# Optimization experiments

Hardware: AMD Instinct MI355X
Metric: run time of the kernel (lower is better)

## Reference

```python
import jax, jax.numpy as jnp
import numpy as np

N = 50000   # nodes
R = 50      # relations
B = 30      # bases
F_IN = 64   # input features
H = 64      # hidden channels
C = 8       # classes
E = 1000000 # edges


def setup_inputs() -> dict:
    key = jax.random.key(0)
    ks = jax.random.split(key, 16)
    x = jax.random.normal(ks[0], (N, F_IN), jnp.float32)
    edge_index = jax.random.randint(ks[1], (2, E), 0, N)
    edge_type = jax.random.randint(ks[2], (E,), 0, R)
    inp = {"x": x, "edge_index": edge_index, "edge_type": edge_type}
    dims = [(F_IN, H), (H, H), (H, C)]
    i = 3
    for l, (din, dout) in enumerate(dims):
        s = 1.0 / np.sqrt(din)
        inp[f"bases{l}"] = jax.random.normal(ks[i], (B, din, dout), jnp.float32) * s; i += 1
        inp[f"comp{l}"] = jax.random.normal(ks[i], (R, B), jnp.float32) / np.sqrt(B); i += 1
        inp[f"root{l}"] = jax.random.normal(ks[i], (din, dout), jnp.float32) * s; i += 1
        inp[f"bias{l}"] = jnp.zeros((dout,), jnp.float32); i += 1
    return inp


def _rgcn(x, bases, comp, root, bias, src, seg):
    # Per-relation mean aggregation (PyG RGCNConv default aggr='mean'):
    # segment id = dst * R + relation. Mean of source features per (dst, rel),
    # then basis-decomposed transform (linearity lets transform follow the mean).
    din = x.shape[1]
    sums = jax.ops.segment_sum(x[src], seg, num_segments=N * R)          # [N*R, din]
    cnt = jax.ops.segment_sum(jnp.ones((seg.shape[0],), x.dtype), seg, num_segments=N * R)
    inv = jnp.where(cnt > 0, 1.0 / jnp.maximum(cnt, 1.0), 0.0)
    agg = (sums * inv[:, None]).reshape(N, R, din)                        # [N, R, din]
    t = jnp.einsum('nri,rb->nbi', agg, comp)                              # [N, B, din]
    msg = jnp.einsum('nbi,bio->no', t, bases)                             # [N, dout]
    return msg + x @ root + bias


def reference(x, edge_index, edge_type,
              bases0, comp0, root0, bias0,
              bases1, comp1, root1, bias1,
              bases2, comp2, root2, bias2):
    src, dst = edge_index[0], edge_index[1]
    seg = dst * R + edge_type
    params = [(bases0, comp0, root0, bias0),
              (bases1, comp1, root1, bias1),
              (bases2, comp2, root2, bias2)]
    x1 = x
    for b, c, r, bi in params:
        x1 = _rgcn(x, b, c, r, bi, src, seg)
        x = jax.nn.relu(x1)
    # original returns log_softmax of the last conv's pre-ReLU output
    return jax.nn.log_softmax(x1, axis=1)
```

## Files before the change

### kernel.cpp

```cpp
#include <hip/hip_runtime.h>
#include <hip/hip_bf16.h>
#include <hip/hip_fp16.h>
#include <stdint.h>

#define NN   50000
#define RR   50
#define BB   30
#define DIN  64
#define EE   1000000
#define KTOT (BB*DIN + DIN)
#define NBW  16
#define ROWE (KTOT + 8)
#define CPAD 32
#define EPAD (EE + 8*NN + 32)

typedef __attribute__((ext_vector_type(8))) short short8;
typedef __attribute__((ext_vector_type(4))) float floatx4;

#define RFL(x) __builtin_amdgcn_readfirstlane(x)


__global__ void k_hist(const int* __restrict__ dst, const int* __restrict__ et,
                       int* __restrict__ cnt) {
    int e = blockIdx.x * 256 + threadIdx.x;
    if (e < EE) {
        int d = dst[e], r = et[e];
        atomicAdd(&cnt[d * RR + r], 1);
    }
}

__global__ void k_scan1(const int* __restrict__ cnt, int* __restrict__ dcount,
                        int* __restrict__ doff, int* __restrict__ bsum) {
    __shared__ int sh[256];
    int t = threadIdx.x;
    int i = blockIdx.x * 256 + t;
    int vp = 0;
    if (i < NN) {
        const int* c = cnt + (size_t)i * RR;
        int v = 0;
#pragma unroll
        for (int r = 0; r < RR; ++r) v += c[r];
        vp = (v + 7) & ~7;
        dcount[i] = vp;
    }
    sh[t] = vp;
    __syncthreads();
    for (int s = 1; s < 256; s <<= 1) {
        int add = (t >= s) ? sh[t - s] : 0;
        __syncthreads();
        sh[t] += add;
        __syncthreads();
    }
    int incl = sh[t];
    if (i < NN) doff[i] = incl - vp;
    if (t == 255) bsum[blockIdx.x] = incl;
}

__global__ void k_scan2(int* __restrict__ bsum, int nbv) {
    __shared__ int sh[256];
    int t = threadIdx.x;
    int v = (t < nbv) ? bsum[t] : 0;
    sh[t] = v;
    __syncthreads();
    for (int s = 1; s < 256; s <<= 1) {
        int add = (t >= s) ? sh[t - s] : 0;
        __syncthreads();
        sh[t] += add;
        __syncthreads();
    }
    if (t < nbv) bsum[t] = sh[t] - v;
}

__global__ void k_scan3(int* __restrict__ doff, const int* __restrict__ bsum) {
    int i = blockIdx.x * 256 + threadIdx.x;
    if (i < NN) doff[i] += bsum[blockIdx.x];
}

__global__ void k_scatter(const int* __restrict__ src, const int* __restrict__ dst,
                          const int* __restrict__ et, const int* __restrict__ cnt,
                          const int* __restrict__ doff, int* __restrict__ cursor,
                          int2* __restrict__ ep2) {
    int e = blockIdx.x * 256 + threadIdx.x;
    if (e < EE) {
        int d = dst[e], r = et[e], s = src[e];
        int p = doff[d] + atomicAdd(&cursor[d], 1);
        float a = 1.0f / (float)cnt[d * RR + r];
        ep2[p] = make_int2(s | (r << 16), __float_as_int(a));
    }
}


__global__ void k_deghist(const int* __restrict__ dcount, int* __restrict__ dbin) {
    __shared__ int lh[256];
    int t = threadIdx.x;
    int i = blockIdx.x * 256 + t;
    lh[t] = 0;
    __syncthreads();
    if (i < NN) {
        int d = dcount[i]; d = (d > 255) ? 255 : d;
        atomicAdd(&lh[255 - d], 1);
    }
    __syncthreads();
    if (lh[t]) atomicAdd(&dbin[t], lh[t]);
}

__global__ void k_degscan(int* __restrict__ dbin) {
    __shared__ int sh[256];
    int t = threadIdx.x;
    int v = dbin[t];
    sh[t] = v;
    __syncthreads();
    for (int s = 1; s < 256; s <<= 1) {
        int add = (t >= s) ? sh[t - s] : 0;
        __syncthreads();
        sh[t] += add;
        __syncthreads();
    }
    dbin[t] = sh[t] - v;
}

__global__ void k_degscatter(const int* __restrict__ dcount, const int* __restrict__ dbin,
                             int* __restrict__ dcur, int* __restrict__ order) {
    __shared__ int lh[256], lbase[256];
    int t = threadIdx.x;
    int i = blockIdx.x * 256 + t;
    lh[t] = 0;
    __syncthreads();
    int b = 0, lpos = 0;
    if (i < NN) {
        int d = dcount[i]; d = (d > 255) ? 255 : d;
        b = 255 - d;
        lpos = atomicAdd(&lh[b], 1);
    }
    __syncthreads();
    lbase[t] = lh[t] ? atomicAdd(&dcur[t], lh[t]) : 0;
    __syncthreads();
    if (i < NN) order[dbin[b] + lbase[b] + lpos] = i;
}

__global__ void k_cast_x(const float* __restrict__ x, __hip_bfloat16* __restrict__ h) {
    int i = blockIdx.x * 256 + threadIdx.x;
    if (i < NN * DIN / 4) {
        float4 v = reinterpret_cast<const float4*>(x)[i];
        ushort4 o;
        o.x = (ushort)(__bfloat16_as_ushort(__float2bfloat16(v.x)));
        o.y = (ushort)(__bfloat16_as_ushort(__float2bfloat16(v.y)));
        o.z = (ushort)(__bfloat16_as_ushort(__float2bfloat16(v.z)));
        o.w = (ushort)(__bfloat16_as_ushort(__float2bfloat16(v.w)));
        reinterpret_cast<ushort4*>(h)[i] = o;
    }
}

__global__ void k_prep_comp3(const float* __restrict__ c0, const float* __restrict__ c1,
                             const float* __restrict__ c2, __half* __restrict__ cp) {
    int idx = blockIdx.x * 256 + threadIdx.x;
    if (idx < 3 * RR * CPAD) {
        int l = idx / (RR * CPAD);
        int rem = idx - l * (RR * CPAD);
        int r = rem / CPAD, i = rem - r * CPAD;
        const float* c = (l == 0) ? c0 : (l == 1) ? c1 : c2;
        cp[idx] = (i < BB) ? __float2half(c[r * BB + i]) : __float2half(0.f);
    }
}

__global__ void k_prep_w3(const float* __restrict__ b0, const float* __restrict__ r0,
                          const float* __restrict__ b1, const float* __restrict__ r1,
                          const float* __restrict__ b2, const float* __restrict__ r2,
                          short* __restrict__ wt) {
    int idx = blockIdx.x * 256 + threadIdx.x;
    if (idx >= 144 * KTOT) return;
    int row = idx / KTOT, k = idx - row * KTOT;
    const float* bs; const float* rt; int o, dout;
    if (row < 64)       { bs = b0; rt = r0; o = row;        dout = 64; }
    else if (row < 128) { bs = b1; rt = r1; o = row - 64;   dout = 64; }
    else                { bs = b2; rt = r2; o = row - 128;  dout = 8;  }
    float v = 0.f;
    if (o < dout)
        v = (k < BB * DIN) ? bs[k * dout + o] : rt[(k - BB * DIN) * dout + o];
    __hip_bfloat16 hb = __float2bfloat16(v);
    wt[idx] = *reinterpret_cast<const short*>(&hb);
}


#define LOADR8(u, R0, R1, R2, R3) do {                                          \
    const int _u = ((u) < nit) ? (u) : (nit - 1);                               \
    R0 = rec4[4 * _u];     R1 = rec4[4 * _u + 1];                               \
    R2 = rec4[4 * _u + 2]; R3 = rec4[4 * _u + 3];                               \
} while (0)

#define GATH1(sx) ((unsigned)xin16[((sx) & 0xFFFF) * DIN + lane])

#define EDGE_FMA1(_sx, _ai, _g) do {                                            \
    const int4* _cr = (const int4*)(compL + (((unsigned)(_sx)) >> 16) * CPAD);  \
    const float _xvf = __uint_as_float((unsigned)(_g) << 16) * __int_as_float(_ai); \
    const __half _xh = __float2half(_xvf);                                      \
    const __half2 _xv2 = __halves2half2(_xh, _xh);                              \
    int4 _m0 = _cr[0], _m1 = _cr[1];                                            \
    {                                                                           \
        const __half2* _p0 = reinterpret_cast<const __half2*>(&_m0);            \
        const __half2* _p1 = reinterpret_cast<const __half2*>(&_m1);            \
        acc[0] = __hfma2(_p0[0], _xv2, acc[0]);                                 \
        acc[1] = __hfma2(_p0[1], _xv2, acc[1]);                                 \
        acc[2] = __hfma2(_p0[2], _xv2, acc[2]);                                 \
        acc[3] = __hfma2(_p0[3], _xv2, acc[3]);                                 \
        acc[4] = __hfma2(_p1[0], _xv2, acc[4]);                                 \
        acc[5] = __hfma2(_p1[1], _xv2, acc[5]);                                 \
        acc[6] = __hfma2(_p1[2], _xv2, acc[6]);                                 \
        acc[7] = __hfma2(_p1[3], _xv2, acc[7]);                                 \
    }                                                                           \
    int4 _m2 = _cr[2], _m3 = _cr[3];                                            \
    {                                                                           \
        const __half2* _p2 = reinterpret_cast<const __half2*>(&_m2);            \
        const __half2* _p3 = reinterpret_cast<const __half2*>(&_m3);            \
        acc[8]  = __hfma2(_p2[0], _xv2, acc[8]);                                \
        acc[9]  = __hfma2(_p2[1], _xv2, acc[9]);                                \
        acc[10] = __hfma2(_p2[2], _xv2, acc[10]);                               \
        acc[11] = __hfma2(_p2[3], _xv2, acc[11]);                               \
        acc[12] = __hfma2(_p3[0], _xv2, acc[12]);                               \
        acc[13] = __hfma2(_p3[1], _xv2, acc[13]);                               \
        acc[14] = __hfma2(_p3[2], _xv2, acc[14]);                               \
        acc[15] = __hfma2(_p3[3], _xv2, acc[15]);                               \
    }                                                                           \
    __builtin_amdgcn_sched_barrier(0);                                          \
} while (0)

template <int DOUT, bool RELU>
__global__ __launch_bounds__(1024, 8)
void k_fused(const __hip_bfloat16* __restrict__ xin,
             const int2* __restrict__ ep2,
             const int* __restrict__ doff, const int* __restrict__ dcount,
             const int* __restrict__ order,
             const __half* __restrict__ compH,
             const short* __restrict__ Wt,
             const float* __restrict__ bias,
             void* __restrict__ outp) {
    __shared__ __align__(16) char smem_raw[NBW * ROWE * 2];
    __shared__ __align__(16) __half compL[RR * CPAD];
    auto t_tile = reinterpret_cast<__hip_bfloat16(*)[ROWE]>(smem_raw);
    const unsigned short* xin16 = reinterpret_cast<const unsigned short*>(xin);
    const int tid  = threadIdx.x;
    const int lane = tid & 63;
    const int wv   = RFL(tid >> 6);
    const int node0 = blockIdx.x * NBW;

    if (tid < RR * CPAD / 2)
        reinterpret_cast<__half2*>(compL)[tid] =
            reinterpret_cast<const __half2*>(compH)[tid];

    const int n   = RFL(order[node0 + wv]);
    const int beg = RFL(doff[n]);
    const int nit = RFL(dcount[n]) >> 3;
    const unsigned selfb = GATH1(n);

    __syncthreads();

    {
        __half2 acc[16];
#pragma unroll
        for (int u = 0; u < 16; ++u)
            acc[u] = __halves2half2(__float2half(0.f), __float2half(0.f));

        if (nit > 0) {
            const int4* rec4 = (const int4*)(ep2 + beg);
            int4 A0, A1, A2, A3, B0, B1, B2, B3;
            LOADR8(0, A0, A1, A2, A3);
            LOADR8(1, B0, B1, B2, B3);
            unsigned g0 = GATH1(RFL(A0.x)), g1 = GATH1(RFL(A0.z));
            unsigned g2 = GATH1(RFL(A1.x)), g3 = GATH1(RFL(A1.z));
            unsigned g4 = GATH1(RFL(A2.x)), g5 = GATH1(RFL(A2.z));
            unsigned g6 = GATH1(RFL(A3.x)), g7 = GATH1(RFL(A3.z));

            for (int t = 0; t < nit; ++t) {
                unsigned h0 = GATH1(RFL(B0.x)), h1 = GATH1(RFL(B0.z));
                unsigned h2 = GATH1(RFL(B1.x)), h3 = GATH1(RFL(B1.z));
                unsigned h4 = GATH1(RFL(B2.x)), h5 = GATH1(RFL(B2.z));
                unsigned h6 = GATH1(RFL(B3.x)), h7 = GATH1(RFL(B3.z));
                EDGE_FMA1(RFL(A0.x), RFL(A0.y), g0);
                EDGE_FMA1(RFL(A0.z), RFL(A0.w), g1);
                EDGE_FMA1(RFL(A1.x), RFL(A1.y), g2);
                EDGE_FMA1(RFL(A1.z), RFL(A1.w), g3);
                EDGE_FMA1(RFL(A2.x), RFL(A2.y), g4);
                EDGE_FMA1(RFL(A2.z), RFL(A2.w), g5);
                EDGE_FMA1(RFL(A3.x), RFL(A3.y), g6);
                EDGE_FMA1(RFL(A3.z), RFL(A3.w), g7);
                A0 = B0; A1 = B1; A2 = B2; A3 = B3;
                LOADR8(t + 2, B0, B1, B2, B3);
                g0 = h0; g1 = h1; g2 = h2; g3 = h3;
                g4 = h4; g5 = h5; g6 = h6; g7 = h7;
            }
        }
#pragma unroll
        for (int b = 0; b < BB; ++b) {
            const float v = (b & 1) ? __high2float(acc[b >> 1]) : __low2float(acc[b >> 1]);
            t_tile[wv][b * DIN + lane] = __float2bfloat16(v);
        }
        t_tile[wv][BB * DIN + lane] =
            __float2bfloat16(__uint_as_float(selfb << 16));
    }
    __syncthreads();

    const int m = lane & 15;
    const int q = lane >> 4;
    int kk0, nsteps, col_base, kpart;
    if (DOUT == 64) {
        kpart = wv >> 2;
        col_base = (wv & 3) * 16;
        kk0    = (kpart <= 1) ? kpart * 16 : (kpart == 2 ? 32 : 47);
        nsteps = (kpart <= 1) ? 16 : 15;
    } else {
        kpart = wv;
        col_base = 0;
        kk0    = (kpart < 14) ? kpart * 4 : (kpart == 14 ? 56 : 59);
        nsteps = (kpart < 14) ? 4 : 3;
    }
    const __hip_bfloat16* arow = &t_tile[m][q * 8];
    const short* brow = Wt + (size_t)(col_base + m) * KTOT + q * 8;

    floatx4 acc0 = {0.f, 0.f, 0.f, 0.f};
    floatx4 acc1 = {0.f, 0.f, 0.f, 0.f};
    int s = 0;
    for (; s + 2 <= nsteps; s += 2) {
        const int kk = kk0 + s;
        short8 a0 = *reinterpret_cast<const short8*>(arow + kk * 32);
        short8 b0 = *reinterpret_cast<const short8*>(brow + kk * 32);
        short8 a1 = *reinterpret_cast<const short8*>(arow + (kk + 1) * 32);
        short8 b1 = *reinterpret_cast<const short8*>(brow + (kk + 1) * 32);
        acc0 = __builtin_amdgcn_mfma_f32_16x16x32_bf16(a0, b0, acc0, 0, 0, 0);
        acc1 = __builtin_amdgcn_mfma_f32_16x16x32_bf16(a1, b1, acc1, 0, 0, 0);
    }
    if (s < nsteps) {
        const int kk = kk0 + s;
        short8 a0 = *reinterpret_cast<const short8*>(arow + kk * 32);
        short8 b0 = *reinterpret_cast<const short8*>(brow + kk * 32);
        acc0 = __builtin_amdgcn_mfma_f32_16x16x32_bf16(a0, b0, acc0, 0, 0, 0);
    }
    floatx4 P = acc0 + acc1;

    __syncthreads();
    float* red = (float*)smem_raw;

    if (DOUT == 64) {
        if (kpart > 0) {
            const int slot = (wv & 3) * 3 + (kpart - 1);
            const int off = (slot * 64 + lane) * 6;
            red[off] = P[0]; red[off + 1] = P[1]; red[off + 2] = P[2]; red[off + 3] = P[3];
        }
        __syncthreads();
        if (kpart == 0) {
#pragma unroll
            for (int t = 0; t < 3; ++t) {
                const int off = (((wv & 3) * 3 + t) * 64 + lane) * 6;
                P[0] += red[off]; P[1] += red[off + 1];
                P[2] += red[off + 2]; P[3] += red[off + 3];
            }
            const int o = col_base + m;
            const float bi = bias[o];
#pragma unroll
            for (int r = 0; r < 4; ++r) {
                const int nw = order[node0 + q * 4 + r];
                float v = P[r] + bi;
                if (RELU) {
                    v = fmaxf(v, 0.f);
                    reinterpret_cast<__hip_bfloat16*>(outp)[(size_t)nw * DOUT + o] =
                        __float2bfloat16(v);
                } else {
                    reinterpret_cast<float*>(outp)[(size_t)nw * DOUT + o] = v;
                }
            }
        }
    } else {
        if (kpart > 0) {
            const int off = ((kpart - 1) * 64 + lane) * 6;
            red[off] = P[0]; red[off + 1] = P[1]; red[off + 2] = P[2]; red[off + 3] = P[3];
        }
        __syncthreads();
        if (kpart == 0) {
#pragma unroll
            for (int w = 0; w < 15; ++w) {
                const int off = (w * 64 + lane) * 6;
                P[0] += red[off]; P[1] += red[off + 1];
                P[2] += red[off + 2]; P[3] += red[off + 3];
            }
            if (m < DOUT) {
                const int o = m;
                const float bi = bias[o];
#pragma unroll
                for (int r = 0; r < 4; ++r) {
                    const int nw = order[node0 + q * 4 + r];
                    reinterpret_cast<float*>(outp)[(size_t)nw * DOUT + o] = P[r] + bi;
                }
            }
        }
    }
}

__global__ void k_lsm(const float* __restrict__ pre, float* __restrict__ out) {
    int n = blockIdx.x * 256 + threadIdx.x;
    if (n < NN) {
        float v[8];
        float mx = -1e30f;
#pragma unroll
        for (int c = 0; c < 8; ++c) { v[c] = pre[n * 8 + c]; mx = fmaxf(mx, v[c]); }
        float s = 0.f;
#pragma unroll
        for (int c = 0; c < 8; ++c) s += expf(v[c] - mx);
        float ls = logf(s);
#pragma unroll
        for (int c = 0; c < 8; ++c) out[n * 8 + c] = v[c] - mx - ls;
    }
}

extern "C" void kernel_launch(void* const* d_in, const int* in_sizes, int n_in,
                              void* d_out, int out_size, void* d_ws, size_t ws_size,
                              hipStream_t stream) {
    const float* x     = (const float*)d_in[0];
    const int*   eidx  = (const int*)d_in[1];
    const int*   etype = (const int*)d_in[2];
    const float* bases0 = (const float*)d_in[3];
    const float* comp0  = (const float*)d_in[4];
    const float* root0  = (const float*)d_in[5];
    const float* bias0  = (const float*)d_in[6];
    const float* bases1 = (const float*)d_in[7];
    const float* comp1  = (const float*)d_in[8];
    const float* root1  = (const float*)d_in[9];
    const float* bias1  = (const float*)d_in[10];
    const float* bases2 = (const float*)d_in[11];
    const float* comp2  = (const float*)d_in[12];
    const float* root2  = (const float*)d_in[13];
    const float* bias2  = (const float*)d_in[14];
    const int* srcp = eidx;
    const int* dstp = eidx + EE;

    char* p = (char*)d_ws;
    auto carve = [&](size_t bytes) -> char* {
        char* r = p;
        p += (bytes + 255) & ~(size_t)255;
        return r;
    };
    int*  cnt    = (int*)carve((size_t)NN * RR * sizeof(int));
    int*  dcount = (int*)carve((size_t)NN * sizeof(int));
    int*  cursor = (int*)carve((size_t)NN * sizeof(int));
    int*  doff   = (int*)carve((size_t)NN * sizeof(int));
    int*  bsum   = (int*)carve(256 * sizeof(int));
    int*  dbin   = (int*)carve(256 * sizeof(int));
    int*  dcur   = (int*)carve(256 * sizeof(int));
    int*  order  = (int*)carve((size_t)NN * sizeof(int));
    int2* ep2    = (int2*)carve((size_t)EPAD * sizeof(int2));
    __hip_bfloat16* h0 = (__hip_bfloat16*)carve((size_t)NN * DIN * 2);
    __hip_bfloat16* h1 = (__hip_bfloat16*)carve((size_t)NN * DIN * 2);
    __hip_bfloat16* h2 = (__hip_bfloat16*)carve((size_t)NN * DIN * 2);
    float* pre = (float*)carve((size_t)NN * 8 * sizeof(float));
    short* wtA = (short*)carve((size_t)144 * KTOT * sizeof(short));
    __half* cpA = (__half*)carve((size_t)3 * RR * CPAD * sizeof(__half));

    hipMemsetAsync(cnt, 0, (size_t)NN * (RR + 2) * sizeof(int) + 512, stream);
    hipMemsetAsync(dbin, 0, 2048, stream);
    hipMemsetAsync(ep2, 0, (size_t)EPAD * sizeof(int2), stream);

    const int EB = (EE + 255) / 256;
    const int NB = (NN + 255) / 256;
    k_hist<<<EB, 256, 0, stream>>>(dstp, etype, cnt);
    k_scan1<<<NB, 256, 0, stream>>>(cnt, dcount, doff, bsum);
    k_scan2<<<1, 256, 0, stream>>>(bsum, NB);
    k_scan3<<<NB, 256, 0, stream>>>(doff, bsum);
    k_scatter<<<EB, 256, 0, stream>>>(srcp, dstp, etype, cnt, doff, cursor, ep2);
    k_deghist<<<NB, 256, 0, stream>>>(dcount, dbin);
    k_degscan<<<1, 256, 0, stream>>>(dbin);
    k_degscatter<<<NB, 256, 0, stream>>>(dcount, dbin, dcur, order);
    k_cast_x<<<(NN * DIN / 4 + 255) / 256, 256, 0, stream>>>(x, h0);
    k_prep_comp3<<<(3 * RR * CPAD + 255) / 256, 256, 0, stream>>>(comp0, comp1, comp2, cpA);
    k_prep_w3<<<(144 * KTOT + 255) / 256, 256, 0, stream>>>(bases0, root0, bases1, root1,
                                                            bases2, root2, wtA);

    short* wt0 = wtA;
    short* wt1 = wtA + (size_t)64 * KTOT;
    short* wt2 = wtA + (size_t)128 * KTOT;
    __half* cp0 = cpA;
    __half* cp1 = cpA + RR * CPAD;
    __half* cp2 = cpA + 2 * RR * CPAD;

    const int NF = NN / NBW;
    k_fused<64, true ><<<NF, 1024, 0, stream>>>(h0, ep2, doff, dcount, order, cp0, wt0, bias0, (void*)h1);
    k_fused<64, true ><<<NF, 1024, 0, stream>>>(h1, ep2, doff, dcount, order, cp1, wt1, bias1, (void*)h2);
    k_fused<8,  false><<<NF, 1024, 0, stream>>>(h2, ep2, doff, dcount, order, cp2, wt2, bias2, (void*)pre);
    k_lsm<<<NB, 256, 0, stream>>>(pre, (float*)d_out);
}
```

Baseline: 563.8 us.

## Process two edges per wave with half-wave lanes handling two features each

Restructures the edge aggregation loop so the wave splits into two halves. Each half takes a different edge of a pair, and each lane gathers two bf16 features with one 32-bit load. Lanes keep two sets of accumulators, one per feature, and the halves are combined at the end with a cross-lane shuffle before packing to bf16 in the tile. The aim is to halve the per-edge instruction count and gather load count. The cost is doubled accumulator registers, the extra shuffle reduction, and divergent comp reads from shared memory across the half-waves.

```diff
diff --git a/kernel.cpp b/kernel.cpp
--- a/kernel.cpp
+++ b/kernel.cpp
@@ -188,38 +188,71 @@
     R2 = rec4[4 * _u + 2]; R3 = rec4[4 * _u + 3];                               \
 } while (0)
 
-#define GATH1(sx) ((unsigned)xin16[((sx) & 0xFFFF) * DIN + lane])
-
-#define EDGE_FMA1(_sx, _ai, _g) do {                                            \
-    const int4* _cr = (const int4*)(compL + (((unsigned)(_sx)) >> 16) * CPAD);  \
-    const float _xvf = __uint_as_float((unsigned)(_g) << 16) * __int_as_float(_ai); \
-    const __half _xh = __float2half(_xvf);                                      \
-    const __half2 _xv2 = __halves2half2(_xh, _xh);                              \
-    int4 _m0 = _cr[0], _m1 = _cr[1];                                            \
+#define GPAIR(RA, g) do {                                                       \
+    const int _sA = RFL((RA).x) & 0xFFFF;                                       \
+    const int _sB = RFL((RA).z) & 0xFFFF;                                       \
+    const int _s  = lo ? _sA : _sB;                                             \
+    g = *(const unsigned*)(xc + (size_t)_s * 128 + lanef4);                     \
+} while (0)
+
+#define PAIR_FMA(RA, _g) do {                                                   \
+    const int _relA = RFL((RA).x) >> 16, _relB = RFL((RA).z) >> 16;             \
+    const int _aiA  = RFL((RA).y),       _aiB  = RFL((RA).w);                   \
+    const int _rel  = lo ? _relA : _relB;                                       \
+    const float _as = __int_as_float(lo ? _aiA : _aiB);                         \
+    const __half2* _cp = (const __half2*)(compL + (_rel & 63) * CPAD);          \
+    const float _f0 = __uint_as_float(((_g) & 0xFFFFu) << 16) * _as;            \
+    const float _f1 = __uint_as_float((_g) & 0xFFFF0000u) * _as;                \
+    const __half _h0 = __float2half(_f0), _h1 = __float2half(_f1);              \
+    const __half2 _x0 = __halves2half2(_h0, _h0);                               \
+    const __half2 _x1 = __halves2half2(_h1, _h1);                               \
     {                                                                           \
-        const __half2* _p0 = reinterpret_cast<const __half2*>(&_m0);            \
-        const __half2* _p1 = reinterpret_cast<const __half2*>(&_m1);            \
-        acc[0] = __hfma2(_p0[0], _xv2, acc[0]);                                 \
-        acc[1] = __hfma2(_p0[1], _xv2, acc[1]);                                 \
-        acc[2] = __hfma2(_p0[2], _xv2, acc[2]);                                 \
-        acc[3] = __hfma2(_p0[3], _xv2, acc[3]);                                 \
-        acc[4] = __hfma2(_p1[0], _xv2, acc[4]);                                 \
-        acc[5] = __hfma2(_p1[1], _xv2, acc[5]);                                 \
-        acc[6] = __hfma2(_p1[2], _xv2, acc[6]);                                 \
-        acc[7] = __hfma2(_p1[3], _xv2, acc[7]);                                 \
+        int4 _m = *(const int4*)(_cp);                                          \
+        const __half2* _c2 = (const __half2*)&_m;                               \
+        accA[0] = __hfma2(_c2[0], _x0, accA[0]);                                \
+        accB[0] = __hfma2(_c2[0], _x1, accB[0]);                                \
+        accA[1] = __hfma2(_c2[1], _x0, accA[1]);                                \
+        accB[1] = __hfma2(_c2[1], _x1, accB[1]);                                \
+        accA[2] = __hfma2(_c2[2], _x0, accA[2]);                                \
+        accB[2] = __hfma2(_c2[2], _x1, accB[2]);                                \
+        accA[3] = __hfma2(_c2[3], _x0, accA[3]);                                \
+        accB[3] = __hfma2(_c2[3], _x1, accB[3]);                                \
     }                                                                           \
-    int4 _m2 = _cr[2], _m3 = _cr[3];                                            \
     {                                                                           \
-        const __half2* _p2 = reinterpret_cast<const __half2*>(&_m2);            \
-        const __half2* _p3 = reinterpret_cast<const __half2*>(&_m3);            \
-        acc[8]  = __hfma2(_p2[0], _xv2, acc[8]);                                \
-        acc[9]  = __hfma2(_p2[1], _xv2, acc[9]);                                \
-        acc[10] = __hfma2(_p2[2], _xv2, acc[10]);                               \
-        acc[11] = __hfma2(_p2[3], _xv2, acc[11]);                               \
-        acc[12] = __hfma2(_p3[0], _xv2, acc[12]);                               \
-        acc[13] = __hfma2(_p3[1], _xv2, acc[13]);                               \
-        acc[14] = __hfma2(_p3[2], _xv2, acc[14]);                               \
-        acc[15] = __hfma2(_p3[3], _xv2, acc[15]);                               \
+        int4 _m = *(const int4*)(_cp + 4);                                      \
+        const __half2* _c2 = (const __half2*)&_m;                               \
+        accA[4] = __hfma2(_c2[0], _x0, accA[4]);                                \
+        accB[4] = __hfma2(_c2[0], _x1, accB[4]);                                \
+        accA[5] = __hfma2(_c2[1], _x0, accA[5]);                                \
+        accB[5] = __hfma2(_c2[1], _x1, accB[5]);                                \
+        accA[6] = __hfma2(_c2[2], _x0, accA[6]);                                \
+        accB[6] = __hfma2(_c2[2], _x1, accB[6]);                                \
+        accA[7] = __hfma2(_c2[3], _x0, accA[7]);                                \
+        accB[7] = __hfma2(_c2[3], _x1, accB[7]);                                \
+    }                                                                           \
+    {                                                                           \
+        int4 _m = *(const int4*)(_cp + 8);                                      \
+        const __half2* _c2 = (const __half2*)&_m;                               \
+        accA[8]  = __hfma2(_c2[0], _x0, accA[8]);                               \
+        accB[8]  = __hfma2(_c2[0], _x1, accB[8]);                               \
+        accA[9]  = __hfma2(_c2[1], _x0, accA[9]);                               \
+        accB[9]  = __hfma2(_c2[1], _x1, accB[9]);                               \
+        accA[10] = __hfma2(_c2[2], _x0, accA[10]);                              \
+        accB[10] = __hfma2(_c2[2], _x1, accB[10]);                              \
+        accA[11] = __hfma2(_c2[3], _x0, accA[11]);                              \
+        accB[11] = __hfma2(_c2[3], _x1, accB[11]);                              \
+    }                                                                           \
+    {                                                                           \
+        int4 _m = *(const int4*)(_cp + 12);                                     \
+        const __half2* _c2 = (const __half2*)&_m;                               \
+        accA[12] = __hfma2(_c2[0], _x0, accA[12]);                              \
+        accB[12] = __hfma2(_c2[0], _x1, accB[12]);                              \
+        accA[13] = __hfma2(_c2[1], _x0, accA[13]);                              \
+        accB[13] = __hfma2(_c2[1], _x1, accB[13]);                              \
+        accA[14] = __hfma2(_c2[2], _x0, accA[14]);                              \
+        accB[14] = __hfma2(_c2[2], _x1, accB[14]);                              \
+        accA[15] = __hfma2(_c2[3], _x0, accA[15]);                              \
+        accB[15] = __hfma2(_c2[3], _x1, accB[15]);                              \
     }                                                                           \
     __builtin_amdgcn_sched_barrier(0);                                          \
 } while (0)
@@ -238,8 +271,11 @@
     __shared__ __align__(16) __half compL[RR * CPAD];
     auto t_tile = reinterpret_cast<__hip_bfloat16(*)[ROWE]>(smem_raw);
     const unsigned short* xin16 = reinterpret_cast<const unsigned short*>(xin);
+    const char* xc = reinterpret_cast<const char*>(xin);
     const int tid  = threadIdx.x;
     const int lane = tid & 63;
+    const bool lo  = lane < 32;
+    const int lanef4 = (lane & 31) * 4;
     const int wv   = RFL(tid >> 6);
     const int node0 = blockIdx.x * NBW;
 
@@ -250,49 +286,55 @@
     const int n   = RFL(order[node0 + wv]);
     const int beg = RFL(doff[n]);
     const int nit = RFL(dcount[n]) >> 3;
-    const unsigned selfb = GATH1(n);
+    const unsigned selfb = (unsigned)xin16[n * DIN + lane];
 
     __syncthreads();
 
     {
-        __half2 acc[16];
-#pragma unroll
-        for (int u = 0; u < 16; ++u)
-            acc[u] = __halves2half2(__float2half(0.f), __float2half(0.f));
+        __half2 accA[16], accB[16];
+#pragma unroll
+        for (int u = 0; u < 16; ++u) {
+            accA[u] = __halves2half2(__float2half(0.f), __float2half(0.f));
+            accB[u] = __halves2half2(__float2half(0.f), __float2half(0.f));
+        }
 
         if (nit > 0) {
             const int4* rec4 = (const int4*)(ep2 + beg);
             int4 A0, A1, A2, A3, B0, B1, B2, B3;
             LOADR8(0, A0, A1, A2, A3);
             LOADR8(1, B0, B1, B2, B3);
-            unsigned g0 = GATH1(RFL(A0.x)), g1 = GATH1(RFL(A0.z));
-            unsigned g2 = GATH1(RFL(A1.x)), g3 = GATH1(RFL(A1.z));
-            unsigned g4 = GATH1(RFL(A2.x)), g5 = GATH1(RFL(A2.z));
-            unsigned g6 = GATH1(RFL(A3.x)), g7 = GATH1(RFL(A3.z));
+            unsigned g0, g1, g2, g3;
+            GPAIR(A0, g0); GPAIR(A1, g1); GPAIR(A2, g2); GPAIR(A3, g3);
 
             for (int t = 0; t < nit; ++t) {
-                unsigned h0 = GATH1(RFL(B0.x)), h1 = GATH1(RFL(B0.z));
-                unsigned h2 = GATH1(RFL(B1.x)), h3 = GATH1(RFL(B1.z));
-                unsigned h4 = GATH1(RFL(B2.x)), h5 = GATH1(RFL(B2.z));
-                unsigned h6 = GATH1(RFL(B3.x)), h7 = GATH1(RFL(B3.z));
-                EDGE_FMA1(RFL(A0.x), RFL(A0.y), g0);
-                EDGE_FMA1(RFL(A0.z), RFL(A0.w), g1);
-                EDGE_FMA1(RFL(A1.x), RFL(A1.y), g2);
-                EDGE_FMA1(RFL(A1.z), RFL(A1.w), g3);
-                EDGE_FMA1(RFL(A2.x), RFL(A2.y), g4);
-                EDGE_FMA1(RFL(A2.z), RFL(A2.w), g5);
-                EDGE_FMA1(RFL(A3.x), RFL(A3.y), g6);
-                EDGE_FMA1(RFL(A3.z), RFL(A3.w), g7);
+                unsigned n0, n1, n2, n3;
+                GPAIR(B0, n0); GPAIR(B1, n1); GPAIR(B2, n2); GPAIR(B3, n3);
+                PAIR_FMA(A0, g0); PAIR_FMA(A1, g1);
+                PAIR_FMA(A2, g2); PAIR_FMA(A3, g3);
                 A0 = B0; A1 = B1; A2 = B2; A3 = B3;
                 LOADR8(t + 2, B0, B1, B2, B3);
-                g0 = h0; g1 = h1; g2 = h2; g3 = h3;
-                g4 = h4; g5 = h5; g6 = h6; g7 = h7;
+                g0 = n0; g1 = n1; g2 = n2; g3 = n3;
             }
         }
 #pragma unroll
-        for (int b = 0; b < BB; ++b) {
-            const float v = (b & 1) ? __high2float(acc[b >> 1]) : __low2float(acc[b >> 1]);
-            t_tile[wv][b * DIN + lane] = __float2bfloat16(v);
+        for (int k = 0; k < 15; ++k) {
+            int va = *reinterpret_cast<int*>(&accA[k]);
+            int vb = *reinterpret_cast<int*>(&accB[k]);
+            int oa = __shfl_xor(va, 32);
+            int ob = __shfl_xor(vb, 32);
+            __half2 sA = __hadd2(accA[k], *reinterpret_cast<__half2*>(&oa));
+            __half2 sB = __hadd2(accB[k], *reinterpret_cast<__half2*>(&ob));
+            if (lo) {
+                const int f0 = 2 * lane;
+                unsigned p0 =
+                    ((unsigned)__bfloat16_as_ushort(__float2bfloat16(__low2float(sA)))) |
+                    (((unsigned)__bfloat16_as_ushort(__float2bfloat16(__low2float(sB)))) << 16);
+                unsigned p1 =
+                    ((unsigned)__bfloat16_as_ushort(__float2bfloat16(__high2float(sA)))) |
+                    (((unsigned)__bfloat16_as_ushort(__float2bfloat16(__high2float(sB)))) << 16);
+                *reinterpret_cast<unsigned*>(&t_tile[wv][(2 * k) * DIN + f0]) = p0;
+                *reinterpret_cast<unsigned*>(&t_tile[wv][(2 * k + 1) * DIN + f0]) = p1;
+            }
         }
         t_tile[wv][BB * DIN + lane] =
             __float2bfloat16(__uint_as_float(selfb << 16));
```

Result: slower. 585.2 us (+3.8%).
